# Kernel tuning notes

Measured on AMD Instinct MI355X. Metric: run time of the kernel, lower is better.

Reference implementation:

```python
import jax, jax.numpy as jnp
import numpy as np

WS = 8          # window_size
POOL = 7        # int(sqrt(agent_num=49)) -> AdaptiveAvgPool1d output size


def _pool_matrix(L, p):
    """Averaging matrix [L, p] replicating torch AdaptiveAvgPool1d(L -> p)."""
    starts = np.floor(np.arange(p) * L / p).astype(int)
    ends = np.ceil((np.arange(p) + 1) * L / p).astype(int)
    P = np.zeros((L, p), dtype=np.float32)
    for i in range(p):
        P[starts[i]:ends[i], i] = 1.0 / (ends[i] - starts[i])
    return jnp.asarray(P)


def setup_inputs() -> dict:
    key = jax.random.key(0)
    ks = jax.random.split(key, 4)
    B, C, H, W = 8, 96, 192, 192
    s = 1.0 / np.sqrt(C)
    return {
        "x": jax.random.normal(ks[0], (B, C, H, W), jnp.float32),
        "Wv": jax.random.normal(ks[1], (C, C), jnp.float32) * s,
        "bv": jnp.zeros((C,), jnp.float32),
        "Wq": jax.random.normal(ks[2], (C, C), jnp.float32) * s,
        "bq": jnp.zeros((C,), jnp.float32),
        "Wk": jax.random.normal(ks[3], (C, C), jnp.float32) * s,
        "bk": jnp.zeros((C,), jnp.float32),
    }


def _conv1x1(x, Wt, b):
    # Conv2d(dim, dim, 1): weight [out, in]
    return jnp.einsum('bchw,oc->bohw', x, Wt) + b[None, :, None, None]


def reference(x, Wv, bv, Wq, bq, Wk, bk):
    B, C, H, W = x.shape
    ws = WS
    nh, nw = H // ws, W // ws
    L = ws * ws  # tokens per window (64)

    v = _conv1x1(x, Wv, bv)
    q = _conv1x1(x, Wq, bq)
    k = _conv1x1(x, Wk, bk)

    def win(t):  # b c (h dh) (w dw) -> (b h w) (dh dw) c
        t = t.reshape(B, C, nh, ws, nw, ws)
        return t.transpose(0, 2, 4, 3, 5, 1).reshape(B * nh * nw, L, C)

    vw, qw, kw = win(v), win(q), win(k)  # (N, 64, C) each

    # agent tokens: adaptive avg pool over the 64 in-window positions -> 7
    P = _pool_matrix(L, POOL)
    agent = jnp.einsum('nlc,lp->npc', qw, P)  # (N, 7, C)

    # agent attention (attn_drop = 0 -> identity)
    a_attn = jax.nn.softmax(jnp.einsum('npc,nlc->npl', agent, kw), axis=-1)
    agent_v = jnp.einsum('npl,nlc->npc', a_attn, vw)            # (N, 7, C)
    q_attn = jax.nn.softmax(jnp.einsum('nlc,npc->nlp', qw, agent), axis=-1)
    f = jnp.einsum('nlp,npc->nlc', q_attn, agent_v)             # (N, 64, C)

    # (b h w) (dh dw) c -> b c (h dh) (w dw)
    out = f.reshape(B, nh, nw, ws, ws, C).transpose(0, 5, 1, 3, 2, 4)
    return out.reshape(B, C, H, W)
```

## Files before the change

kernel.cpp:

```cpp
#include <hip/hip_runtime.h>


constexpr int C_   = 96;
constexpr int Wimg = 192;
constexpr int HWp  = 192 * 192;
constexpr int NWIN = 24;
constexpr int Pp   = 7;

typedef __attribute__((ext_vector_type(8))) __bf16 bf16x8;
typedef __attribute__((ext_vector_type(4))) __bf16 bf16x4;
typedef __attribute__((ext_vector_type(8))) short  short8;
typedef __attribute__((ext_vector_type(4))) float  f32x4;
union frag_u { short8 s; bf16x8 b; };

constexpr int XWS   = 0;
constexpr int XPH   = 12288;
constexpr int XPL   = 13888;
constexpr int GKA   = 15488;
constexpr int GKQH  = GKA;
constexpr int GKQL  = GKA + 3200;
constexpr int AVH   = GKA;
constexpr int AVL   = GKA + 3072;
constexpr int QATH  = 21888;
constexpr int QATL  = 24448;
constexpr int LRAW  = 27008;
constexpr int BIAS  = 31232;
constexpr int SMEMB = 31296;

constexpr int WS_FRAG_BYTE = 18944 * 4;
constexpr int WS_WV_BYTE   = WS_FRAG_BYTE + 84 * 1024;


__device__ __forceinline__ void bar() {
    asm volatile("s_waitcnt lgkmcnt(0)" ::: "memory");
    __builtin_amdgcn_s_barrier();
}

__device__ __forceinline__ short8 xws_fragA(const unsigned char* S, int mt, int ks, int lane) {
    const int c  = mt * 16 + (lane & 15);
    const int l2 = ks * 64 + ((lane >> 4) << 4);
    return *reinterpret_cast<const short8*>(S + XWS + c * 128 + (l2 ^ ((c & 7) << 4)));
}

__device__ __forceinline__ void put_hilo(unsigned char* S, int hi_off, int lo_off, float v) {
    const __bf16 h = (__bf16)v;
    *reinterpret_cast<__bf16*>(S + hi_off) = h;
    *reinterpret_cast<__bf16*>(S + lo_off) = (__bf16)(v - (float)h);
}


__global__ void precompute_mats(const float* __restrict__ Wq,
                                const float* __restrict__ Wk,
                                float* __restrict__ Mk,
                                float* __restrict__ Mq)
{
    const int c  = blockIdx.x;
    const int cp = threadIdx.x;
    float ak = 0.f, aq = 0.f;
    for (int a = 0; a < C_; ++a) {
        const float wq = Wq[a * C_ + c];
        ak = fmaf(wq, Wk[a * C_ + cp], ak);
        aq = fmaf(wq, Wq[a * C_ + cp], aq);
    }
    Mk[c * C_ + cp] = ak;
    Mq[c * C_ + cp] = aq;
}

__global__ void precompute_vecs(const float* __restrict__ Wq,
                                const float* __restrict__ Wk,
                                const float* __restrict__ bq,
                                const float* __restrict__ bk,
                                float* __restrict__ uk,  float* __restrict__ uq,
                                float* __restrict__ bk2, float* __restrict__ bq2,
                                float* __restrict__ scal)
{
    const int c = threadIdx.x;
    float a_uk = 0.f, a_uq = 0.f, a_bk2 = 0.f, a_bq2 = 0.f;
    for (int a = 0; a < C_; ++a) {
        const float wqc = Wq[a * C_ + c];
        a_uk  = fmaf(wqc, bk[a], a_uk);
        a_uq  = fmaf(wqc, bq[a], a_uq);
        a_bk2 = fmaf(bq[a], Wk[a * C_ + c], a_bk2);
        a_bq2 = fmaf(bq[a], Wq[a * C_ + c], a_bq2);
    }
    uk[c] = a_uk; uq[c] = a_uq; bk2[c] = a_bk2; bq2[c] = a_bq2;
    if (c == 0) {
        float sk = 0.f, sq = 0.f;
        for (int a = 0; a < C_; ++a) { sk += bq[a] * bk[a]; sq += bq[a] * bq[a]; }
        scal[0] = sk; scal[1] = sq;
    }
}

__global__ void precompute_frags(const float* __restrict__ ws,
                                 const float* __restrict__ Wv,
                                 unsigned char* __restrict__ wsb)
{
    const int bid = blockIdx.x, lane = threadIdx.x;
    short8 o;
    if (bid < 84) {
        const int hl = bid & 1, ks = (bid >> 1) % 3, nt = (bid / 6) % 7, mat = bid / 42;
        const float* M = ws + (mat ? 9216 : 0);
        const float* u = ws + (mat ? 18528 : 18432);
        const int col = nt * 16 + (lane & 15);
        #pragma unroll
        for (int j = 0; j < 8; ++j) {
            const int k = ks * 32 + (lane >> 4) * 8 + j;
            const float raw = (col < 96) ? M[k * 96 + col] : ((col == 96) ? u[k] : 0.f);
            const __bf16 hi = (__bf16)raw;
            union { __bf16 h; short s; } cv;
            cv.h = hl ? (__bf16)(raw - (float)hi) : hi;
            o[j] = cv.s;
        }
        *reinterpret_cast<short8*>(wsb + WS_FRAG_BYTE + bid * 1024 + lane * 16) = o;
    } else {
        const int wb = bid - 84;
        const int hl = wb & 1, ks = (wb >> 1) % 3, mt = wb / 6;
        const int row = mt * 16 + (lane & 15);
        #pragma unroll
        for (int j = 0; j < 8; ++j) {
            const int c = ks * 32 + (lane >> 4) * 8 + j;
            const float raw = Wv[row * 96 + c];
            const __bf16 hi = (__bf16)raw;
            union { __bf16 h; short s; } cv;
            cv.h = hl ? (__bf16)(raw - (float)hi) : hi;
            o[j] = cv.s;
        }
        *reinterpret_cast<short8*>(wsb + WS_WV_BYTE + wb * 1024 + lane * 16) = o;
    }
}

#define LOADPAIR(dstH, dstL, tab, slot_h) do {                                               \
    (dstH).s = *reinterpret_cast<const short8*>((tab) + (slot_h) * 1024 + (lane << 4));      \
    (dstL).s = *reinterpret_cast<const short8*>((tab) + ((slot_h) + 1) * 1024 + (lane << 4));\
} while (0)


__global__ __launch_bounds__(256, 5) void camixer_main(
    const float* __restrict__ x,
    const float* __restrict__ bv,
    const float* __restrict__ bk2,
    const float* __restrict__ bq2,
    const float* __restrict__ scal,
    const unsigned char* __restrict__ mfrag,
    const unsigned char* __restrict__ wvfrag,
    float* __restrict__ out)
{
    __shared__ __align__(16) unsigned char S[SMEMB];
    float* Lraw   = (float*)(S + LRAW);
    float* bias16 = (float*)(S + BIAS);

    const int t = threadIdx.x;
    const int lane = t & 63, w = t >> 6;
    const int wid = ((blockIdx.x & 7) * 576) + (blockIdx.x >> 3);
    const int b  = wid / (NWIN * NWIN);
    const int r  = wid % (NWIN * NWIN);
    const int h0 = (r / NWIN) * 8;
    const int w0 = (r % NWIN) * 8;
    const int base = b * C_ * HWp + h0 * Wimg + w0;
    const float scal0 = scal[0], scal1 = scal[1];
    const short8 zero8 = {0, 0, 0, 0, 0, 0, 0, 0};

    frag_u B0h[3], B0l[3];
    LOADPAIR(B0h[0], B0l[0], mfrag, (w * 3 + 0) * 2);
    LOADPAIR(B0h[1], B0l[1], mfrag, (w * 3 + 1) * 2);
    LOADPAIR(B0h[2], B0l[2], mfrag, (w * 3 + 2) * 2);

    {
        const float4* x4 = reinterpret_cast<const float4*>(x);
        #pragma unroll
        for (int rr = 0; rr < 2; ++rr) {
            const int idx = t + (rr << 8);
            if (idx < 384) {
                const int dw4 = idx & 1;
                const int dh  = (idx >> 1) & 7;
                const int c4  = idx >> 4;
                const int c0 = c4 * 4, l0 = dh * 8 + dw4 * 4;
                #pragma unroll
                for (int j = 0; j < 4; ++j) {
                    const int c = c0 + j;
                    const float4 v = x4[(base + c * HWp + dh * Wimg + dw4 * 4) >> 2];
                    bf16x4 d = {(__bf16)v.x, (__bf16)v.y, (__bf16)v.z, (__bf16)v.w};
                    *reinterpret_cast<bf16x4*>(S + XWS + c * 128 + ((l0 * 2) ^ ((c & 7) << 4))) = d;
                }
            }
        }
    }
    bar();

    {
        frag_u PAh[2], PAl[2];
        {
            const int p = lane & 15;
            const __bf16 PH = (__bf16)0.1f;
            const __bf16 PL = (__bf16)(0.1f - (float)PH);
            const int sp = (p < 7) ? ((p << 6) / 7) : 1000;
            #pragma unroll
            for (int ks = 0; ks < 2; ++ks)
                #pragma unroll
                for (int j = 0; j < 8; ++j) {
                    const int l = ks * 32 + (lane >> 4) * 8 + j;
                    const bool in = (l >= sp) && (l < sp + 10);
                    PAh[ks].b[j] = in ? PH : (__bf16)0.f;
                    PAl[ks].b[j] = in ? PL : (__bf16)0.f;
                }
        }
        #pragma unroll
        for (int rnd = 0; rnd < 2; ++rnd) {
            const int nt = rnd ? (4 + w) : w;
            if (rnd == 0 || w < 2) {
                f32x4 acc = {0.f, 0.f, 0.f, 0.f};
                #pragma unroll
                for (int ks = 0; ks < 2; ++ks) {
                    frag_u B;
                    B.s = xws_fragA(S, nt, ks, lane);
                    acc = __builtin_amdgcn_mfma_f32_16x16x32_bf16(PAh[ks].b, B.b, acc, 0, 0, 0);
                    acc = __builtin_amdgcn_mfma_f32_16x16x32_bf16(PAl[ks].b, B.b, acc, 0, 0, 0);
                }
                const int cc = nt * 16 + (lane & 15);
                #pragma unroll
                for (int rr = 0; rr < 4; ++rr) {
                    const int p = (lane >> 4) * 4 + rr;
                    if (p < 8)
                        put_hilo(S, XPH + p * 200 + cc * 2, XPL + p * 200 + cc * 2, acc[rr]);
                }
            }
        }
    }
    bar();

    {
        frag_u Ah[3], Al[3];
        #pragma unroll
        for (int ks = 0; ks < 3; ++ks) {
            const int off = ((lane & 15) & 7) * 200 + (ks * 32 + (lane >> 4) * 8) * 2;
            Ah[ks].s = *reinterpret_cast<const short8*>(S + XPH + off);
            Al[ks].s = *reinterpret_cast<const short8*>(S + XPL + off);
        }

        #define G0TILE(TT, BH, BL) do {                                               \
            const int tt_ = (TT);                                                     \
            const int mat_ = (tt_ >= 7) ? 1 : 0;                                      \
            const int nt_  = tt_ - 7 * mat_;                                          \
            f32x4 acc = {0.f, 0.f, 0.f, 0.f};                                         \
            acc = __builtin_amdgcn_mfma_f32_16x16x32_bf16(Ah[0].b, BH[0].b, acc, 0,0,0); \
            acc = __builtin_amdgcn_mfma_f32_16x16x32_bf16(Ah[0].b, BL[0].b, acc, 0,0,0); \
            acc = __builtin_amdgcn_mfma_f32_16x16x32_bf16(Al[0].b, BH[0].b, acc, 0,0,0); \
            acc = __builtin_amdgcn_mfma_f32_16x16x32_bf16(Ah[1].b, BH[1].b, acc, 0,0,0); \
            acc = __builtin_amdgcn_mfma_f32_16x16x32_bf16(Ah[1].b, BL[1].b, acc, 0,0,0); \
            acc = __builtin_amdgcn_mfma_f32_16x16x32_bf16(Al[1].b, BH[1].b, acc, 0,0,0); \
            acc = __builtin_amdgcn_mfma_f32_16x16x32_bf16(Ah[2].b, BH[2].b, acc, 0,0,0); \
            acc = __builtin_amdgcn_mfma_f32_16x16x32_bf16(Ah[2].b, BL[2].b, acc, 0,0,0); \
            acc = __builtin_amdgcn_mfma_f32_16x16x32_bf16(Al[2].b, BH[2].b, acc, 0,0,0); \
            const int row0_ = (lane >> 4) * 4;                                        \
            if (nt_ < 6) {                                                            \
                const int cc_ = nt_ * 16 + (lane & 15);                               \
                const float b2v_ = (mat_ ? bq2 : bk2)[cc_];                           \
                _Pragma("unroll")                                                     \
                for (int rr = 0; rr < 4; ++rr) {                                      \
                    const int rw_ = row0_ + rr;                                       \
                    if (rw_ < 8) {                                                    \
                        const int pr_ = rw_ + 8 * mat_;                               \
                        put_hilo(S, GKQH + pr_ * 200 + cc_ * 2,                       \
                                 GKQL + pr_ * 200 + cc_ * 2, acc[rr] + b2v_);         \
                    }                                                                 \
                }                                                                     \
            } else if ((lane & 15) == 0) {                                            \
                _Pragma("unroll")                                                     \
                for (int rr = 0; rr < 4; ++rr) {                                      \
                    const int rw_ = row0_ + rr;                                       \
                    if (rw_ < 8) bias16[rw_ + 8 * mat_] = acc[rr];                    \
                }                                                                     \
            }                                                                         \
        } while (0)

        frag_u B1h[3], B1l[3], B2h[3], B2l[3], B3h[3], B3l[3];
        LOADPAIR(B1h[0], B1l[0], mfrag, ((w + 4) * 3 + 0) * 2);
        LOADPAIR(B1h[1], B1l[1], mfrag, ((w + 4) * 3 + 1) * 2);
        LOADPAIR(B1h[2], B1l[2], mfrag, ((w + 4) * 3 + 2) * 2);
        G0TILE(w, B0h, B0l);
        LOADPAIR(B2h[0], B2l[0], mfrag, ((w + 8) * 3 + 0) * 2);
        LOADPAIR(B2h[1], B2l[1], mfrag, ((w + 8) * 3 + 1) * 2);
        LOADPAIR(B2h[2], B2l[2], mfrag, ((w + 8) * 3 + 2) * 2);
        G0TILE(w + 4, B1h, B1l);
        if (w < 2) {
            LOADPAIR(B3h[0], B3l[0], mfrag, ((w + 12) * 3 + 0) * 2);
            LOADPAIR(B3h[1], B3l[1], mfrag, ((w + 12) * 3 + 1) * 2);
            LOADPAIR(B3h[2], B3l[2], mfrag, ((w + 12) * 3 + 2) * 2);
        }
        G0TILE(w + 8, B2h, B2l);
        if (w < 2) G0TILE(w + 12, B3h, B3l);
        #undef G0TILE
    }
    bar();

    {
        frag_u B[3];
        {
            const int l2 = (w * 16 + (lane & 15)) * 2;
            const int kb = (lane >> 4) << 10;
            #pragma unroll
            for (int j = 0; j < 8; ++j) {
                const int aj = kb + j * 128 + (l2 ^ (j << 4));
                B[0].b[j] = *reinterpret_cast<const __bf16*>(S + XWS + aj);
                B[1].b[j] = *reinterpret_cast<const __bf16*>(S + XWS + 4096 + aj);
                B[2].b[j] = *reinterpret_cast<const __bf16*>(S + XWS + 8192 + aj);
            }
        }
        frag_u Ah[3], Al[3];
        #pragma unroll
        for (int ks = 0; ks < 3; ++ks) {
            const int off = (lane & 15) * 200 + (ks * 32 + (lane >> 4) * 8) * 2;
            Ah[ks].s = *reinterpret_cast<const short8*>(S + GKQH + off);
            Al[ks].s = *reinterpret_cast<const short8*>(S + GKQL + off);
        }
        f32x4 acc = {0.f, 0.f, 0.f, 0.f};
        #pragma unroll
        for (int ks = 0; ks < 3; ++ks) {
            acc = __builtin_amdgcn_mfma_f32_16x16x32_bf16(Ah[ks].b, B[ks].b, acc, 0, 0, 0);
            acc = __builtin_amdgcn_mfma_f32_16x16x32_bf16(Al[ks].b, B[ks].b, acc, 0, 0, 0);
        }
        const int colL = w * 16 + (lane & 15);
        #pragma unroll
        for (int rr = 0; rr < 4; ++rr) {
            const int pr = (lane >> 4) * 4 + rr;
            Lraw[pr * 66 + colL] = acc[rr] + bias16[pr] + (pr < 8 ? scal0 : scal1);
        }
    }
    bar();

    if (w < 3) {
        #pragma unroll
        for (int rr = 0; rr < 2; ++rr) {
            const int pp = w + 3 * rr;
            const float v = Lraw[pp * 66 + lane];
            float mx = v;
            #pragma unroll
            for (int off = 32; off; off >>= 1) mx = fmaxf(mx, __shfl_xor(mx, off));
            const float e = __expf(v - mx);
            float s = e;
            #pragma unroll
            for (int off = 32; off; off >>= 1) s += __shfl_xor(s, off);
            const float a = e / s;
            const __bf16 hb = (__bf16)a;
            const __bf16 lb = (__bf16)(a - (float)hb);
            const int ks = lane >> 5;
            const int off_b = ((pp + 16 * ((lane >> 3) & 3)) << 4) + ((lane & 7) << 1);
            *reinterpret_cast<__bf16*>(S + GKA + (ks << 10) + off_b) = hb;
            *reinterpret_cast<__bf16*>(S + GKA + ((2 + ks) << 10) + off_b) = lb;
        }
    } else {
        {
            const int pp = 6;
            const float v = Lraw[pp * 66 + lane];
            float mx = v;
            #pragma unroll
            for (int off = 32; off; off >>= 1) mx = fmaxf(mx, __shfl_xor(mx, off));
            const float e = __expf(v - mx);
            float s = e;
            #pragma unroll
            for (int off = 32; off; off >>= 1) s += __shfl_xor(s, off);
            const float a = e / s;
            const __bf16 hb = (__bf16)a;
            const __bf16 lb = (__bf16)(a - (float)hb);
            const int ks = lane >> 5;
            const int off_b = ((pp + 16 * ((lane >> 3) & 3)) << 4) + ((lane & 7) << 1);
            *reinterpret_cast<__bf16*>(S + GKA + (ks << 10) + off_b) = hb;
            *reinterpret_cast<__bf16*>(S + GKA + ((2 + ks) << 10) + off_b) = lb;
        }
        float vv[Pp];
        float mx = -1e30f;
        #pragma unroll
        for (int p = 0; p < Pp; ++p) { vv[p] = Lraw[(8 + p) * 66 + lane]; mx = fmaxf(mx, vv[p]); }
        float s = 0.f;
        #pragma unroll
        for (int p = 0; p < Pp; ++p) { vv[p] = __expf(vv[p] - mx); s += vv[p]; }
        const float inv = 1.f / s;
        frag_u qh, ql;
        #pragma unroll
        for (int p = 0; p < 8; ++p) {
            const float a = (p < Pp) ? vv[p] * inv : 0.f;
            const __bf16 hb = (__bf16)a;
            qh.b[p] = hb;
            ql.b[p] = (__bf16)(a - (float)hb);
        }
        *reinterpret_cast<short8*>(S + QATH + lane * 40)      = qh.s;
        *reinterpret_cast<short8*>(S + QATH + lane * 40 + 16) = zero8;
        *reinterpret_cast<short8*>(S + QATL + lane * 40)      = ql.s;
        *reinterpret_cast<short8*>(S + QATL + lane * 40 + 16) = zero8;
    }
    bar();

    frag_u V0h[3], V0l[3], V1h[3], V1l[3];
    {
        LOADPAIR(V0h[0], V0l[0], wvfrag, (w * 3 + 0) * 2);
        LOADPAIR(V0h[1], V0l[1], wvfrag, (w * 3 + 1) * 2);
        LOADPAIR(V0h[2], V0l[2], wvfrag, (w * 3 + 2) * 2);
        if (w < 2) {
            LOADPAIR(V1h[0], V1l[0], wvfrag, ((4 + w) * 3 + 0) * 2);
            LOADPAIR(V1h[1], V1l[1], wvfrag, ((4 + w) * 3 + 1) * 2);
            LOADPAIR(V1h[2], V1l[2], wvfrag, ((4 + w) * 3 + 2) * 2);
        }

        frag_u Bh[2], Bl[2];
        #pragma unroll
        for (int ks = 0; ks < 2; ++ks) {
            Bh[ks].s = *reinterpret_cast<const short8*>(S + GKA + (ks << 10) + (lane << 4));
            Bl[ks].s = *reinterpret_cast<const short8*>(S + GKA + ((2 + ks) << 10) + (lane << 4));
        }
        const int mt0 = (w < 2) ? w * 2 : (w + 2);
        const int nmt = (w < 2) ? 2 : 1;
        for (int m = 0; m < nmt; ++m) {
            const int mt = mt0 + m;
            f32x4 acc = {0.f, 0.f, 0.f, 0.f};
            #pragma unroll
            for (int ks = 0; ks < 2; ++ks) {
                frag_u A;
                A.s = xws_fragA(S, mt, ks, lane);
                acc = __builtin_amdgcn_mfma_f32_16x16x32_bf16(A.b, Bh[ks].b, acc, 0, 0, 0);
                acc = __builtin_amdgcn_mfma_f32_16x16x32_bf16(A.b, Bl[ks].b, acc, 0, 0, 0);
            }
            const int p = lane & 15;
            if (p < 8) {
                #pragma unroll
                for (int rr = 0; rr < 4; ++rr) {
                    const int c = mt * 16 + (lane >> 4) * 4 + rr;
                    put_hilo(S, XPH + p * 200 + c * 2, XPL + p * 200 + c * 2, acc[rr]);
                }
            }
        }
    }
    bar();

    {
        const bool pok = (lane & 15) < Pp;
        frag_u Bh[3], Bl[3];
        #pragma unroll
        for (int ks = 0; ks < 3; ++ks) {
            const int off = ((lane & 15) & 7) * 200 + (ks * 32 + (lane >> 4) * 8) * 2;
            Bh[ks].s = pok ? *reinterpret_cast<const short8*>(S + XPH + off) : zero8;
            Bl[ks].s = pok ? *reinterpret_cast<const short8*>(S + XPL + off) : zero8;
        }
        #define G3TILE(MT, VH, VL) do {                                               \
            f32x4 acc = {0.f, 0.f, 0.f, 0.f};                                         \
            acc = __builtin_amdgcn_mfma_f32_16x16x32_bf16(VH[0].b, Bh[0].b, acc, 0,0,0); \
            acc = __builtin_amdgcn_mfma_f32_16x16x32_bf16(VH[0].b, Bl[0].b, acc, 0,0,0); \
            acc = __builtin_amdgcn_mfma_f32_16x16x32_bf16(VL[0].b, Bh[0].b, acc, 0,0,0); \
            acc = __builtin_amdgcn_mfma_f32_16x16x32_bf16(VH[1].b, Bh[1].b, acc, 0,0,0); \
            acc = __builtin_amdgcn_mfma_f32_16x16x32_bf16(VH[1].b, Bl[1].b, acc, 0,0,0); \
            acc = __builtin_amdgcn_mfma_f32_16x16x32_bf16(VL[1].b, Bh[1].b, acc, 0,0,0); \
            acc = __builtin_amdgcn_mfma_f32_16x16x32_bf16(VH[2].b, Bh[2].b, acc, 0,0,0); \
            acc = __builtin_amdgcn_mfma_f32_16x16x32_bf16(VH[2].b, Bl[2].b, acc, 0,0,0); \
            acc = __builtin_amdgcn_mfma_f32_16x16x32_bf16(VL[2].b, Bh[2].b, acc, 0,0,0); \
            _Pragma("unroll")                                                         \
            for (int rr = 0; rr < 4; ++rr) {                                          \
                const int o_ = (MT) * 16 + (lane >> 4) * 4 + rr;                      \
                const float v_ = acc[rr] + bv[o_];                                    \
                put_hilo(S, AVH + o_ * 32 + (lane & 15) * 2,                          \
                         AVL + o_ * 32 + (lane & 15) * 2, v_);                        \
            }                                                                         \
        } while (0)
        G3TILE(w, V0h, V0l);
        if (w < 2) G3TILE(4 + w, V1h, V1l);
        #undef G3TILE
    }
    bar();

    {
        const int kblk = lane >> 4, nlow = lane & 15;
        const int l = w * 16 + nlow;
        frag_u Bh, Bl;
        if (kblk < 2) {
            Bh.s = *reinterpret_cast<const short8*>(S + QATH + l * 40 + kblk * 16);
            Bl.s = *reinterpret_cast<const short8*>(S + QATL + l * 40 + kblk * 16);
        } else { Bh.s = zero8; Bl.s = zero8; }
        const int obase = b * C_ * HWp + (h0 + (l >> 3)) * Wimg + w0 + (l & 7);
        #pragma unroll
        for (int mt = 0; mt < 6; ++mt) {
            frag_u Ah, Al;
            if (kblk < 2) {
                Ah.s = *reinterpret_cast<const short8*>(S + AVH + (mt * 16 + nlow) * 32 + kblk * 16);
                Al.s = *reinterpret_cast<const short8*>(S + AVL + (mt * 16 + nlow) * 32 + kblk * 16);
            } else { Ah.s = zero8; Al.s = zero8; }
            f32x4 acc = {0.f, 0.f, 0.f, 0.f};
            acc = __builtin_amdgcn_mfma_f32_16x16x32_bf16(Ah.b, Bh.b, acc, 0, 0, 0);
            acc = __builtin_amdgcn_mfma_f32_16x16x32_bf16(Ah.b, Bl.b, acc, 0, 0, 0);
            acc = __builtin_amdgcn_mfma_f32_16x16x32_bf16(Al.b, Bh.b, acc, 0, 0, 0);
            #pragma unroll
            for (int rr = 0; rr < 4; ++rr) {
                const int o = mt * 16 + kblk * 4 + rr;
                out[obase + o * HWp] = acc[rr];
            }
        }
    }
}


extern "C" void kernel_launch(void* const* d_in, const int* in_sizes, int n_in,
                              void* d_out, int out_size, void* d_ws, size_t ws_size,
                              hipStream_t stream)
{
    const float* x  = (const float*)d_in[0];
    const float* Wv = (const float*)d_in[1];
    const float* bv = (const float*)d_in[2];
    const float* Wq = (const float*)d_in[3];
    const float* bq = (const float*)d_in[4];
    const float* Wk = (const float*)d_in[5];
    const float* bk = (const float*)d_in[6];
    float* out = (float*)d_out;

    float* ws = (float*)d_ws;
    float* Mk   = ws;
    float* Mq   = ws + 9216;
    float* uk   = ws + 18432;
    float* uq   = ws + 18528;
    float* bk2  = ws + 18624;
    float* bq2  = ws + 18720;
    float* scal = ws + 18816;
    unsigned char* wsb = (unsigned char*)d_ws;

    hipLaunchKernelGGL(precompute_mats, dim3(C_), dim3(C_), 0, stream,
                       Wq, Wk, Mk, Mq);
    hipLaunchKernelGGL(precompute_vecs, dim3(1), dim3(C_), 0, stream,
                       Wq, Wk, bq, bk, uk, uq, bk2, bq2, scal);
    hipLaunchKernelGGL(precompute_frags, dim3(120), dim3(64), 0, stream,
                       ws, Wv, wsb);
    hipLaunchKernelGGL(camixer_main, dim3(8 * NWIN * NWIN), dim3(256), 0, stream,
                       x, bv, bk2, bq2, scal,
                       wsb + WS_FRAG_BYTE, wsb + WS_WV_BYTE, out);
}
```

Baseline: 75.38 us.

## Merge precompute kernels, shrink LDS layout, and raise MFMA wave priority

Collapses the three weight-precompute launches into one kernel that computes the Wq^T Wk / Wq^T Wq products inline and writes hi/lo bf16 fragments directly, removing two launches and an intermediate fp32 buffer. The main kernel's shared-memory layout is compacted: the agent-V and q-attention buffers drop their zero-padded halves and the pooled-x and logits regions alias, lowering LDS per block from about 31 KB to 25 KB, which could allow more resident blocks. s_setprio brackets are added around MFMA sequences. The fused precompute does redundant per-lane dot products over 96 elements, which makes it serial and may lengthen that stage.

Result: slower. 82.65 us (+9.6%).

```diff
diff --git a/kernel.cpp b/kernel.cpp
--- a/kernel.cpp
+++ b/kernel.cpp
@@ -14,19 +14,23 @@
 union frag_u { short8 s; bf16x8 b; };
 
 constexpr int XWS   = 0;
-constexpr int XPH   = 12288;
-constexpr int XPL   = 13888;
-constexpr int GKA   = 15488;
-constexpr int GKQH  = GKA;
-constexpr int GKQL  = GKA + 3200;
-constexpr int AVH   = GKA;
-constexpr int AVL   = GKA + 3072;
-constexpr int QATH  = 21888;
-constexpr int QATL  = 24448;
-constexpr int LRAW  = 27008;
-constexpr int BIAS  = 31232;
-constexpr int SMEMB = 31296;
-
+constexpr int RA    = 12288;
+constexpr int XPH   = RA;
+constexpr int XPL   = RA + 1600;
+constexpr int LRAW  = RA;
+constexpr int RB    = 16512;
+constexpr int GKQH  = RB;
+constexpr int GKQL  = RB + 3200;
+constexpr int AVH   = RB;
+constexpr int AVL   = RB + 1536;
+constexpr int QATH  = 22912;
+constexpr int QATL  = 23936;
+constexpr int BIAS  = 24960;
+constexpr int SMEMB = 25024;
+
+constexpr int WS_BK2_F  = 18624;
+constexpr int WS_BQ2_F  = 18720;
+constexpr int WS_SCAL_F = 18816;
 constexpr int WS_FRAG_BYTE = 18944 * 4;
 constexpr int WS_WV_BYTE   = WS_FRAG_BYTE + 84 * 1024;
 
@@ -49,83 +53,78 @@
 }
 
 
-__global__ void precompute_mats(const float* __restrict__ Wq,
-                                const float* __restrict__ Wk,
-                                float* __restrict__ Mk,
-                                float* __restrict__ Mq)
-{
-    const int c  = blockIdx.x;
-    const int cp = threadIdx.x;
-    float ak = 0.f, aq = 0.f;
-    for (int a = 0; a < C_; ++a) {
-        const float wq = Wq[a * C_ + c];
-        ak = fmaf(wq, Wk[a * C_ + cp], ak);
-        aq = fmaf(wq, Wq[a * C_ + cp], aq);
-    }
-    Mk[c * C_ + cp] = ak;
-    Mq[c * C_ + cp] = aq;
-}
-
-__global__ void precompute_vecs(const float* __restrict__ Wq,
-                                const float* __restrict__ Wk,
-                                const float* __restrict__ bq,
-                                const float* __restrict__ bk,
-                                float* __restrict__ uk,  float* __restrict__ uq,
-                                float* __restrict__ bk2, float* __restrict__ bq2,
-                                float* __restrict__ scal)
-{
-    const int c = threadIdx.x;
-    float a_uk = 0.f, a_uq = 0.f, a_bk2 = 0.f, a_bq2 = 0.f;
-    for (int a = 0; a < C_; ++a) {
-        const float wqc = Wq[a * C_ + c];
-        a_uk  = fmaf(wqc, bk[a], a_uk);
-        a_uq  = fmaf(wqc, bq[a], a_uq);
-        a_bk2 = fmaf(bq[a], Wk[a * C_ + c], a_bk2);
-        a_bq2 = fmaf(bq[a], Wq[a * C_ + c], a_bq2);
-    }
-    uk[c] = a_uk; uq[c] = a_uq; bk2[c] = a_bk2; bq2[c] = a_bq2;
-    if (c == 0) {
-        float sk = 0.f, sq = 0.f;
-        for (int a = 0; a < C_; ++a) { sk += bq[a] * bk[a]; sq += bq[a] * bq[a]; }
-        scal[0] = sk; scal[1] = sq;
-    }
-}
-
-__global__ void precompute_frags(const float* __restrict__ ws,
-                                 const float* __restrict__ Wv,
-                                 unsigned char* __restrict__ wsb)
+__global__ void precompute_all(const float* __restrict__ Wq,
+                               const float* __restrict__ Wk,
+                               const float* __restrict__ Wv,
+                               const float* __restrict__ bq,
+                               const float* __restrict__ bk,
+                               float* __restrict__ ws,
+                               unsigned char* __restrict__ wsb)
 {
     const int bid = blockIdx.x, lane = threadIdx.x;
-    short8 o;
-    if (bid < 84) {
-        const int hl = bid & 1, ks = (bid >> 1) % 3, nt = (bid / 6) % 7, mat = bid / 42;
-        const float* M = ws + (mat ? 9216 : 0);
-        const float* u = ws + (mat ? 18528 : 18432);
+    if (bid < 42) {
+        const int mat = bid / 21, rem = bid % 21;
+        const int nt = rem / 3, ks = rem % 3;
+        const float* __restrict__ W2 = mat ? Wq : Wk;
+        const float* __restrict__ bvec = mat ? bq : bk;
         const int col = nt * 16 + (lane & 15);
+        short8 oh, ol;
         #pragma unroll
         for (int j = 0; j < 8; ++j) {
             const int k = ks * 32 + (lane >> 4) * 8 + j;
-            const float raw = (col < 96) ? M[k * 96 + col] : ((col == 96) ? u[k] : 0.f);
+            float raw = 0.f;
+            if (col < 96) {
+                for (int a = 0; a < C_; ++a)
+                    raw = fmaf(Wq[a * C_ + k], W2[a * C_ + col], raw);
+            } else if (col == 96) {
+                for (int a = 0; a < C_; ++a)
+                    raw = fmaf(Wq[a * C_ + k], bvec[a], raw);
+            }
             const __bf16 hi = (__bf16)raw;
             union { __bf16 h; short s; } cv;
-            cv.h = hl ? (__bf16)(raw - (float)hi) : hi;
-            o[j] = cv.s;
-        }
-        *reinterpret_cast<short8*>(wsb + WS_FRAG_BYTE + bid * 1024 + lane * 16) = o;
-    } else {
-        const int wb = bid - 84;
-        const int hl = wb & 1, ks = (wb >> 1) % 3, mt = wb / 6;
+            cv.h = hi; oh[j] = cv.s;
+            cv.h = (__bf16)(raw - (float)hi); ol[j] = cv.s;
+        }
+        const int slot = ((mat * 7 + nt) * 3 + ks) * 2;
+        *reinterpret_cast<short8*>(wsb + WS_FRAG_BYTE + slot * 1024 + lane * 16) = oh;
+        *reinterpret_cast<short8*>(wsb + WS_FRAG_BYTE + (slot + 1) * 1024 + lane * 16) = ol;
+    } else if (bid < 60) {
+        const int wb = bid - 42;
+        const int mt = wb / 3, ks = wb % 3;
         const int row = mt * 16 + (lane & 15);
+        short8 oh, ol;
         #pragma unroll
         for (int j = 0; j < 8; ++j) {
             const int c = ks * 32 + (lane >> 4) * 8 + j;
-            const float raw = Wv[row * 96 + c];
+            const float raw = Wv[row * C_ + c];
             const __bf16 hi = (__bf16)raw;
             union { __bf16 h; short s; } cv;
-            cv.h = hl ? (__bf16)(raw - (float)hi) : hi;
-            o[j] = cv.s;
-        }
-        *reinterpret_cast<short8*>(wsb + WS_WV_BYTE + wb * 1024 + lane * 16) = o;
+            cv.h = hi; oh[j] = cv.s;
+            cv.h = (__bf16)(raw - (float)hi); ol[j] = cv.s;
+        }
+        const int slot = (mt * 3 + ks) * 2;
+        *reinterpret_cast<short8*>(wsb + WS_WV_BYTE + slot * 1024 + lane * 16) = oh;
+        *reinterpret_cast<short8*>(wsb + WS_WV_BYTE + (slot + 1) * 1024 + lane * 16) = ol;
+    } else {
+        #pragma unroll
+        for (int it = 0; it < 2; ++it) {
+            const int c = lane + it * 64;
+            if (c < 96) {
+                float a_bk2 = 0.f, a_bq2 = 0.f;
+                for (int a = 0; a < C_; ++a) {
+                    a_bk2 = fmaf(bq[a], Wk[a * C_ + c], a_bk2);
+                    a_bq2 = fmaf(bq[a], Wq[a * C_ + c], a_bq2);
+                }
+                ws[WS_BK2_F + c] = a_bk2;
+                ws[WS_BQ2_F + c] = a_bq2;
+            }
+        }
+        if (lane == 0) {
+            float sk = 0.f, sq = 0.f;
+            for (int a = 0; a < C_; ++a) { sk += bq[a] * bk[a]; sq += bq[a] * bq[a]; }
+            ws[WS_SCAL_F]     = sk;
+            ws[WS_SCAL_F + 1] = sq;
+        }
     }
 }
 
@@ -209,6 +208,7 @@
             const int nt = rnd ? (4 + w) : w;
             if (rnd == 0 || w < 2) {
                 f32x4 acc = {0.f, 0.f, 0.f, 0.f};
+                __builtin_amdgcn_s_setprio(1);
                 #pragma unroll
                 for (int ks = 0; ks < 2; ++ks) {
                     frag_u B;
@@ -216,6 +216,7 @@
                     acc = __builtin_amdgcn_mfma_f32_16x16x32_bf16(PAh[ks].b, B.b, acc, 0, 0, 0);
                     acc = __builtin_amdgcn_mfma_f32_16x16x32_bf16(PAl[ks].b, B.b, acc, 0, 0, 0);
                 }
+                __builtin_amdgcn_s_setprio(0);
                 const int cc = nt * 16 + (lane & 15);
                 #pragma unroll
                 for (int rr = 0; rr < 4; ++rr) {
@@ -242,6 +243,7 @@
             const int mat_ = (tt_ >= 7) ? 1 : 0;                                      \
             const int nt_  = tt_ - 7 * mat_;                                          \
             f32x4 acc = {0.f, 0.f, 0.f, 0.f};                                         \
+            __builtin_amdgcn_s_setprio(1);                                            \
             acc = __builtin_amdgcn_mfma_f32_16x16x32_bf16(Ah[0].b, BH[0].b, acc, 0,0,0); \
             acc = __builtin_amdgcn_mfma_f32_16x16x32_bf16(Ah[0].b, BL[0].b, acc, 0,0,0); \
             acc = __builtin_amdgcn_mfma_f32_16x16x32_bf16(Al[0].b, BH[0].b, acc, 0,0,0); \
@@ -251,6 +253,7 @@
             acc = __builtin_amdgcn_mfma_f32_16x16x32_bf16(Ah[2].b, BH[2].b, acc, 0,0,0); \
             acc = __builtin_amdgcn_mfma_f32_16x16x32_bf16(Ah[2].b, BL[2].b, acc, 0,0,0); \
             acc = __builtin_amdgcn_mfma_f32_16x16x32_bf16(Al[2].b, BH[2].b, acc, 0,0,0); \
+            __builtin_amdgcn_s_setprio(0);                                            \
             const int row0_ = (lane >> 4) * 4;                                        \
             if (nt_ < 6) {                                                            \
                 const int cc_ = nt_ * 16 + (lane & 15);                               \
@@ -314,11 +317,13 @@
             Al[ks].s = *reinterpret_cast<const short8*>(S + GKQL + off);
         }
         f32x4 acc = {0.f, 0.f, 0.f, 0.f};
+        __builtin_amdgcn_s_setprio(1);
         #pragma unroll
         for (int ks = 0; ks < 3; ++ks) {
             acc = __builtin_amdgcn_mfma_f32_16x16x32_bf16(Ah[ks].b, B[ks].b, acc, 0, 0, 0);
             acc = __builtin_amdgcn_mfma_f32_16x16x32_bf16(Al[ks].b, B[ks].b, acc, 0, 0, 0);
         }
+        __builtin_amdgcn_s_setprio(0);
         const int colL = w * 16 + (lane & 15);
         #pragma unroll
         for (int rr = 0; rr < 4; ++rr) {
@@ -345,8 +350,8 @@
             const __bf16 lb = (__bf16)(a - (float)hb);
             const int ks = lane >> 5;
             const int off_b = ((pp + 16 * ((lane >> 3) & 3)) << 4) + ((lane & 7) << 1);
-            *reinterpret_cast<__bf16*>(S + GKA + (ks << 10) + off_b) = hb;
-            *reinterpret_cast<__bf16*>(S + GKA + ((2 + ks) << 10) + off_b) = lb;
+            *reinterpret_cast<__bf16*>(S + RB + (ks << 10) + off_b) = hb;
+            *reinterpret_cast<__bf16*>(S + RB + ((2 + ks) << 10) + off_b) = lb;
         }
     } else {
         {
@@ -364,8 +369,8 @@
             const __bf16 lb = (__bf16)(a - (float)hb);
             const int ks = lane >> 5;
             const int off_b = ((pp + 16 * ((lane >> 3) & 3)) << 4) + ((lane & 7) << 1);
-            *reinterpret_cast<__bf16*>(S + GKA + (ks << 10) + off_b) = hb;
-            *reinterpret_cast<__bf16*>(S + GKA + ((2 + ks) << 10) + off_b) = lb;
+            *reinterpret_cast<__bf16*>(S + RB + (ks << 10) + off_b) = hb;
+            *reinterpret_cast<__bf16*>(S + RB + ((2 + ks) << 10) + off_b) = lb;
         }
         float vv[Pp];
         float mx = -1e30f;
@@ -383,10 +388,8 @@
             qh.b[p] = hb;
             ql.b[p] = (__bf16)(a - (float)hb);
         }
-        *reinterpret_cast<short8*>(S + QATH + lane * 40)      = qh.s;
-        *reinterpret_cast<short8*>(S + QATH + lane * 40 + 16) = zero8;
-        *reinterpret_cast<short8*>(S + QATL + lane * 40)      = ql.s;
-        *reinterpret_cast<short8*>(S + QATL + lane * 40 + 16) = zero8;
+        *reinterpret_cast<short8*>(S + QATH + lane * 16) = qh.s;
+        *reinterpret_cast<short8*>(S + QATL + lane * 16) = ql.s;
     }
     bar();
 
@@ -404,14 +407,15 @@
         frag_u Bh[2], Bl[2];
         #pragma unroll
         for (int ks = 0; ks < 2; ++ks) {
-            Bh[ks].s = *reinterpret_cast<const short8*>(S + GKA + (ks << 10) + (lane << 4));
-            Bl[ks].s = *reinterpret_cast<const short8*>(S + GKA + ((2 + ks) << 10) + (lane << 4));
+            Bh[ks].s = *reinterpret_cast<const short8*>(S + RB + (ks << 10) + (lane << 4));
+            Bl[ks].s = *reinterpret_cast<const short8*>(S + RB + ((2 + ks) << 10) + (lane << 4));
         }
         const int mt0 = (w < 2) ? w * 2 : (w + 2);
         const int nmt = (w < 2) ? 2 : 1;
         for (int m = 0; m < nmt; ++m) {
             const int mt = mt0 + m;
             f32x4 acc = {0.f, 0.f, 0.f, 0.f};
+            __builtin_amdgcn_s_setprio(1);
             #pragma unroll
             for (int ks = 0; ks < 2; ++ks) {
                 frag_u A;
@@ -419,6 +423,7 @@
                 acc = __builtin_amdgcn_mfma_f32_16x16x32_bf16(A.b, Bh[ks].b, acc, 0, 0, 0);
                 acc = __builtin_amdgcn_mfma_f32_16x16x32_bf16(A.b, Bl[ks].b, acc, 0, 0, 0);
             }
+            __builtin_amdgcn_s_setprio(0);
             const int p = lane & 15;
             if (p < 8) {
                 #pragma unroll
@@ -442,6 +447,7 @@
         }
         #define G3TILE(MT, VH, VL) do {                                               \
             f32x4 acc = {0.f, 0.f, 0.f, 0.f};                                         \
+            __builtin_amdgcn_s_setprio(1);                                            \
             acc = __builtin_amdgcn_mfma_f32_16x16x32_bf16(VH[0].b, Bh[0].b, acc, 0,0,0); \
             acc = __builtin_amdgcn_mfma_f32_16x16x32_bf16(VH[0].b, Bl[0].b, acc, 0,0,0); \
             acc = __builtin_amdgcn_mfma_f32_16x16x32_bf16(VL[0].b, Bh[0].b, acc, 0,0,0); \
@@ -451,12 +457,15 @@
             acc = __builtin_amdgcn_mfma_f32_16x16x32_bf16(VH[2].b, Bh[2].b, acc, 0,0,0); \
             acc = __builtin_amdgcn_mfma_f32_16x16x32_bf16(VH[2].b, Bl[2].b, acc, 0,0,0); \
             acc = __builtin_amdgcn_mfma_f32_16x16x32_bf16(VL[2].b, Bh[2].b, acc, 0,0,0); \
-            _Pragma("unroll")                                                         \
-            for (int rr = 0; rr < 4; ++rr) {                                          \
-                const int o_ = (MT) * 16 + (lane >> 4) * 4 + rr;                      \
-                const float v_ = acc[rr] + bv[o_];                                    \
-                put_hilo(S, AVH + o_ * 32 + (lane & 15) * 2,                          \
-                         AVL + o_ * 32 + (lane & 15) * 2, v_);                        \
+            __builtin_amdgcn_s_setprio(0);                                            \
+            if ((lane & 15) < 8) {                                                    \
+                _Pragma("unroll")                                                     \
+                for (int rr = 0; rr < 4; ++rr) {                                      \
+                    const int o_ = (MT) * 16 + (lane >> 4) * 4 + rr;                  \
+                    const float v_ = acc[rr] + bv[o_];                                \
+                    put_hilo(S, AVH + o_ * 16 + (lane & 15) * 2,                      \
+                             AVL + o_ * 16 + (lane & 15) * 2, v_);                    \
+                }                                                                     \
             }                                                                         \
         } while (0)
         G3TILE(w, V0h, V0l);
@@ -469,22 +478,24 @@
         const int kblk = lane >> 4, nlow = lane & 15;
         const int l = w * 16 + nlow;
         frag_u Bh, Bl;
-        if (kblk < 2) {
-            Bh.s = *reinterpret_cast<const short8*>(S + QATH + l * 40 + kblk * 16);
-            Bl.s = *reinterpret_cast<const short8*>(S + QATL + l * 40 + kblk * 16);
+        if (kblk == 0) {
+            Bh.s = *reinterpret_cast<const short8*>(S + QATH + l * 16);
+            Bl.s = *reinterpret_cast<const short8*>(S + QATL + l * 16);
         } else { Bh.s = zero8; Bl.s = zero8; }
         const int obase = b * C_ * HWp + (h0 + (l >> 3)) * Wimg + w0 + (l & 7);
         #pragma unroll
         for (int mt = 0; mt < 6; ++mt) {
             frag_u Ah, Al;
-            if (kblk < 2) {
-                Ah.s = *reinterpret_cast<const short8*>(S + AVH + (mt * 16 + nlow) * 32 + kblk * 16);
-                Al.s = *reinterpret_cast<const short8*>(S + AVL + (mt * 16 + nlow) * 32 + kblk * 16);
+            if (kblk == 0) {
+                Ah.s = *reinterpret_cast<const short8*>(S + AVH + (mt * 16 + nlow) * 16);
+                Al.s = *reinterpret_cast<const short8*>(S + AVL + (mt * 16 + nlow) * 16);
             } else { Ah.s = zero8; Al.s = zero8; }
             f32x4 acc = {0.f, 0.f, 0.f, 0.f};
+            __builtin_amdgcn_s_setprio(1);
             acc = __builtin_amdgcn_mfma_f32_16x16x32_bf16(Ah.b, Bh.b, acc, 0, 0, 0);
             acc = __builtin_amdgcn_mfma_f32_16x16x32_bf16(Ah.b, Bl.b, acc, 0, 0, 0);
             acc = __builtin_amdgcn_mfma_f32_16x16x32_bf16(Al.b, Bh.b, acc, 0, 0, 0);
+            __builtin_amdgcn_s_setprio(0);
             #pragma unroll
             for (int rr = 0; rr < 4; ++rr) {
                 const int o = mt * 16 + kblk * 4 + rr;
@@ -509,22 +520,11 @@
     float* out = (float*)d_out;
 
     float* ws = (float*)d_ws;
-    float* Mk   = ws;
-    float* Mq   = ws + 9216;
-    float* uk   = ws + 18432;
-    float* uq   = ws + 18528;
-    float* bk2  = ws + 18624;
-    float* bq2  = ws + 18720;
-    float* scal = ws + 18816;
     unsigned char* wsb = (unsigned char*)d_ws;
 
-    hipLaunchKernelGGL(precompute_mats, dim3(C_), dim3(C_), 0, stream,
-                       Wq, Wk, Mk, Mq);
-    hipLaunchKernelGGL(precompute_vecs, dim3(1), dim3(C_), 0, stream,
-                       Wq, Wk, bq, bk, uk, uq, bk2, bq2, scal);
-    hipLaunchKernelGGL(precompute_frags, dim3(120), dim3(64), 0, stream,
-                       ws, Wv, wsb);
+    hipLaunchKernelGGL(precompute_all, dim3(61), dim3(64), 0, stream,
+                       Wq, Wk, Wv, bq, bk, ws, wsb);
     hipLaunchKernelGGL(camixer_main, dim3(8 * NWIN * NWIN), dim3(256), 0, stream,
-                       x, bv, bk2, bq2, scal,
+                       x, bv, ws + WS_BK2_F, ws + WS_BQ2_F, ws + WS_SCAL_F,
                        wsb + WS_FRAG_BYTE, wsb + WS_WV_BYTE, out);
 }
```
